# Kernel tuning notes

Measured on AMD Instinct MI355X. Metric: run time of the kernel, lower is better.

Reference implementation:

```python
import jax, jax.numpy as jnp
import numpy as np

V = 32          # num_variables
T = 48          # num_time_bins
D = 512         # d_model
H = 8           # num_heads
HD = D // H     # head_dim = 64
OD = 16         # observation_dim
B = 4


def setup_inputs() -> dict:
    key = jax.random.key(0)
    ks = jax.random.split(key, 20)
    s = 0.02
    inp = {
        'h': jax.random.normal(ks[0], (B, T, V, D), jnp.float32),
        'observation_state': jax.random.normal(ks[1], (B, T, V, 2), jnp.float32),
        'Wq': jax.random.normal(ks[2], (D, D), jnp.float32) * s,
        'bq': jnp.zeros((D,), jnp.float32),
        'Wk': jax.random.normal(ks[3], (D, D), jnp.float32) * s,
        'bk': jnp.zeros((D,), jnp.float32),
        'Wv': jax.random.normal(ks[4], (D, D), jnp.float32) * s,
        'bv': jnp.zeros((D,), jnp.float32),
        'Wo': jax.random.normal(ks[5], (D, D), jnp.float32) * s,
        'bo': jnp.zeros((D,), jnp.float32),
        'Woq': jax.random.normal(ks[6], (2, H * OD), jnp.float32) * 0.5,
        'boq': jnp.zeros((H * OD,), jnp.float32),
        'Wok': jax.random.normal(ks[7], (2, H * OD), jnp.float32) * 0.5,
        'bok': jnp.zeros((H * OD,), jnp.float32),
        'variable_bias': jax.random.normal(ks[8], (H, V, V), jnp.float32) * 0.01,
        'relative_time_bias': jax.random.normal(ks[9], (H, 2 * T - 1), jnp.float32) * 0.01,
    }
    return inp


def reference(h, observation_state, Wq, bq, Wk, bk, Wv, bv, Wo, bo,
              Woq, boq, Wok, bok, variable_bias, relative_time_bias):
    N = T * V
    scale = 1.0 / np.sqrt(HD)
    obs_scale = 1.0 / np.sqrt(OD)

    # static index buffers (constants)
    flat_var_ids = jnp.tile(jnp.arange(V), T)                       # [N]
    flat_time_ids = jnp.repeat(jnp.arange(T), V)                    # [N]
    rel_index = flat_time_ids[:, None] - flat_time_ids[None, :] + (T - 1)  # [N,N]

    fh = h.reshape(B, N, D)
    fo = observation_state.reshape(B, N, 2)

    def heads(x, nh, hd):
        return x.reshape(B, N, nh, hd).transpose(0, 2, 1, 3)  # [B,H,N,hd]

    q = heads(fh @ Wq + bq, H, HD)
    k = heads(fh @ Wk + bk, H, HD)
    v = heads(fh @ Wv + bv, H, HD)
    oq = heads(fo @ Woq + boq, H, OD)
    ok = heads(fo @ Wok + bok, H, OD)

    content = jnp.einsum('bhnd,bhmd->bhnm', q, k) * scale
    obs = jnp.einsum('bhnd,bhmd->bhnm', oq, ok) * obs_scale
    var_scores = variable_bias[:, flat_var_ids[:, None], flat_var_ids[None, :]]  # [H,N,N]
    time_scores = relative_time_bias[:, rel_index]                                # [H,N,N]

    scores = content + obs + var_scores[None] + time_scores[None]
    attn = jax.nn.softmax(scores, axis=-1)  # dropout off (inference)
    out = jnp.einsum('bhnm,bhmd->bhnd', attn, v)
    out = out.transpose(0, 2, 1, 3).reshape(B, N, D)
    out = out @ Wo + bo
    return out.reshape(B, T, V, D)
```

## Files before the change

### kernel.cpp

```cpp
#include <hip/hip_runtime.h>
#include <math.h>

typedef __bf16 bf16x8 __attribute__((ext_vector_type(8)));
typedef float f32x4 __attribute__((ext_vector_type(4)));

#define NB 4
#define NT 48
#define NV 32
#define ND 512
#define NH 8
#define NN 1536
#define NBN 6144
#define L2E 1.44269504f

#define GLOAD_LDS(g, l) \
    __builtin_amdgcn_global_load_lds( \
        (const __attribute__((address_space(1))) void*)(g), \
        (__attribute__((address_space(3))) void*)(l), 16, 0, 0)

__global__ __launch_bounds__(256) void prep(
    const float* __restrict__ h, const float* __restrict__ obs,
    const float* __restrict__ Wq, const float* __restrict__ Wk,
    const float* __restrict__ Wv, const float* __restrict__ Wo,
    const float* __restrict__ bq, const float* __restrict__ bk,
    const float* __restrict__ bv,
    const float* __restrict__ Wok, const float* __restrict__ bok,
    __bf16* __restrict__ h_bf, __bf16* __restrict__ WcatT,
    __bf16* __restrict__ WoT, float* __restrict__ biascat,
    __bf16* __restrict__ kx)
{
    __shared__ float ts[64][68];
    const int tid = threadIdx.x;
    const int bx = blockIdx.x;
    if (bx < 1536) {
        int t = bx * 256 + tid;
        const float4* src = (const float4*)h + (size_t)t * 2;
        float4 a = src[0], b = src[1];
        __bf16 r[8] = {(__bf16)a.x, (__bf16)a.y, (__bf16)a.z, (__bf16)a.w,
                       (__bf16)b.x, (__bf16)b.y, (__bf16)b.z, (__bf16)b.w};
        *(uint4*)(h_bf + (size_t)t * 8) = *(uint4*)r;
    } else if (bx < 1792) {
        int bw = bx - 1536;
        const int p = bw >> 6, tile = bw & 63;
        const int k0 = (tile >> 3) * 64, c0 = (tile & 7) * 64;
        const float* W = (p == 0) ? Wq : (p == 1) ? Wk : (p == 2) ? Wv : Wo;
        const float scale = (p == 0) ? 0.125f * L2E : 1.0f;
        #pragma unroll
        for (int i = 0; i < 4; i++) {
            int r = (tid >> 4) + i * 16;
            float4 v = *(const float4*)(W + (size_t)(k0 + r) * 512 + c0 + (tid & 15) * 4);
            *(float4*)&ts[r][(tid & 15) * 4] = v;
        }
        __syncthreads();
        __bf16 tmp[16];
        #pragma unroll
        for (int j = 0; j < 16; j++)
            tmp[j] = (__bf16)(ts[(tid & 3) * 16 + j][tid >> 2] * scale);
        int crow = c0 + (tid >> 2);
        __bf16* dst = (p < 3)
            ? WcatT + ((size_t)(p * 512 + crow)) * 512 + k0 + (tid & 3) * 16
            : WoT   + ((size_t)crow) * 512 + k0 + (tid & 3) * 16;
        *(uint4*)dst = *(uint4*)tmp;
        *(uint4*)(dst + 8) = *(uint4*)(tmp + 8);
        if (p < 3 && k0 == 0 && tid < 64) {
            const float* bb = (p == 0) ? bq : (p == 1) ? bk : bv;
            biascat[p * 512 + c0 + tid] = bb[c0 + tid] * scale;
        }
    } else {
        int t = (bx - 1792) * 256 + tid;
        int row = t >> 1, half = t & 1;
        __bf16* dst = kx + (size_t)row * 96 + 64 + half * 16;
        if (half == 0) {
            int bh = row / NN, n = row - bh * NN;
            int b = bh >> 3, hh = bh & 7;
            size_t bn = (size_t)b * NN + n;
            float o0 = obs[bn * 2], o1 = obs[bn * 2 + 1];
            int f = hh * 16;
            __bf16 tmp[16];
            #pragma unroll
            for (int j = 0; j < 16; j++)
                tmp[j] = (__bf16)(o0 * Wok[f + j] + o1 * Wok[128 + f + j] + bok[f + j]);
            *(uint4*)dst       = *(uint4*)tmp;
            *(uint4*)(dst + 8) = *(uint4*)(tmp + 8);
        } else {
            uint4 z = {0, 0, 0, 0};
            *(uint4*)dst       = z;
            *(uint4*)(dst + 8) = z;
        }
    }
}

template<int TM, bool BF16OUT>
__global__ __launch_bounds__(256) void gemm_mfma(
    const __bf16* __restrict__ A, const __bf16* __restrict__ Bt,
    const float* __restrict__ bias, float* __restrict__ Cf,
    __bf16* __restrict__ qarr, __bf16* __restrict__ kx,
    __bf16* __restrict__ vt)
{
    constexpr int MT = TM / 32;
    __shared__ __align__(16) char smem[34816];
    __bf16 (*As)[32] = (__bf16(*)[32])smem;
    __bf16 (*Bs)[32] = (__bf16(*)[32])(smem + TM * 64);
    const int tid = threadIdx.x;
    const int w = tid >> 6, lane = tid & 63;
    const int quad = lane >> 4, l16 = lane & 15;
    const int wm = w >> 1, wn = w & 1;
    const int n0 = blockIdx.x * 128, m0 = blockIdx.y * TM;

    const int sm = tid >> 2;
    const int sk = ((tid & 3) ^ ((sm >> 1) & 3)) * 8;
    const __bf16* aptr = A  + (size_t)(m0 + sm) * 512 + sk;
    const __bf16* bptr = Bt + (size_t)(n0 + sm) * 512 + sk;
    __bf16* lA = (__bf16*)As + tid * 8;
    __bf16* lB = (__bf16*)Bs + tid * 8;

    f32x4 zero4 = {0.f, 0.f, 0.f, 0.f};
    f32x4 acc[MT][4];
    #pragma unroll
    for (int i = 0; i < MT; i++)
        #pragma unroll
        for (int j = 0; j < 4; j++) acc[i][j] = zero4;

    for (int kt = 0; kt < 512; kt += 32) {
        __syncthreads();
        GLOAD_LDS(aptr + kt, lA);
        if (TM == 128) GLOAD_LDS(aptr + 64 * 512 + kt, lA + 2048);
        GLOAD_LDS(bptr + kt, lB);
        GLOAD_LDS(bptr + 64 * 512 + kt, lB + 2048);
        __syncthreads();
        bf16x8 af[MT], bfr[4];
        #pragma unroll
        for (int mt = 0; mt < MT; mt++) {
            int rr = wm * (TM / 2) + mt * 16 + l16;
            af[mt] = *(const bf16x8*)&As[rr][(quad ^ ((rr >> 1) & 3)) * 8];
        }
        #pragma unroll
        for (int nt = 0; nt < 4; nt++) {
            int rr = wn * 64 + nt * 16 + l16;
            bfr[nt] = *(const bf16x8*)&Bs[rr][(quad ^ ((rr >> 1) & 3)) * 8];
        }
        #pragma unroll
        for (int mt = 0; mt < MT; mt++)
            #pragma unroll
            for (int nt = 0; nt < 4; nt++)
                acc[mt][nt] = __builtin_amdgcn_mfma_f32_16x16x32_bf16(
                    af[mt], bfr[nt], acc[mt][nt], 0, 0, 0);
    }

    __syncthreads();
    if (BF16OUT) {
        if (n0 >= 1024) {
            __bf16* CsT = (__bf16*)smem;
            #pragma unroll
            for (int nt = 0; nt < 4; nt++) {
                int cl = wn * 64 + nt * 16 + l16;
                float bia = bias[n0 + cl];
                #pragma unroll
                for (int mt = 0; mt < MT; mt++) {
                    int rl0 = wm * (TM / 2) + mt * 16 + quad * 4;
                    __bf16 pk[4];
                    #pragma unroll
                    for (int r = 0; r < 4; r++)
                        pk[r] = (__bf16)(acc[mt][nt][r] + bia);
                    *(uint2*)&CsT[cl * 136 + rl0] = *(uint2*)pk;
                }
            }
            __syncthreads();
            int cl = tid >> 1, half = tid & 1;
            int f0 = (n0 + cl) & 511;
            int hh = f0 >> 6, d = f0 & 63;
            int bidx = m0 / NN, nm = m0 - bidx * NN;
            __bf16* dst = vt + ((size_t)(bidx * 8 + hh) * 64 + d) * 1536
                             + nm + half * 64;
            #pragma unroll
            for (int j = 0; j < 8; j++) {
                uint4 v = *(uint4*)&CsT[cl * 136 + half * 64 + j * 8];
                *(uint4*)(dst + j * 8) = v;
            }
        } else {
            __bf16* Cs = (__bf16*)smem;
            #pragma unroll
            for (int mt = 0; mt < MT; mt++)
                #pragma unroll
                for (int nt = 0; nt < 4; nt++) {
                    int cl = wn * 64 + nt * 16 + l16;
                    float bia = bias[n0 + cl];
                    #pragma unroll
                    for (int r = 0; r < 4; r++) {
                        int rl = wm * (TM / 2) + mt * 16 + quad * 4 + r;
                        Cs[rl * 132 + cl] = (__bf16)(acc[mt][nt][r] + bia);
                    }
                }
            __syncthreads();
            int rl = tid >> 1, hb = tid & 1;
            int grow = m0 + rl;
            int col0 = n0 + hb * 64;
            int p = col0 >> 9, f0 = col0 & 511, hh = f0 >> 6;
            int bidx = grow / NN, n = grow - bidx * NN;
            __bf16* dst = (p == 0) ? qarr + (size_t)grow * 512 + f0
                                   : kx + ((size_t)(bidx * 8 + hh) * NN + n) * 96;
            #pragma unroll
            for (int j = 0; j < 8; j++) {
                uint2 lo = *(uint2*)&Cs[rl * 132 + hb * 64 + j * 8];
                uint2 hi = *(uint2*)&Cs[rl * 132 + hb * 64 + j * 8 + 4];
                uint4 v = {lo.x, lo.y, hi.x, hi.y};
                *(uint4*)(dst + j * 8) = v;
            }
        }
    } else {
        float* Csf = (float*)smem;
        #pragma unroll
        for (int mt = 0; mt < MT; mt++)
            #pragma unroll
            for (int nt = 0; nt < 4; nt++) {
                int cl = wn * 64 + nt * 16 + l16;
                float bia = bias[n0 + cl];
                #pragma unroll
                for (int r = 0; r < 4; r++) {
                    int rl = wm * (TM / 2) + mt * 16 + quad * 4 + r;
                    Csf[rl * 132 + cl] = acc[mt][nt][r] + bia;
                }
            }
        __syncthreads();
        int rl = tid >> 2, q4 = tid & 3;
        float* dst = Cf + (size_t)(m0 + rl) * 512 + n0 + q4 * 32;
        #pragma unroll
        for (int j = 0; j < 8; j++) {
            uint4 v = *(uint4*)&Csf[rl * 132 + q4 * 32 + j * 4];
            *(uint4*)(dst + j * 4) = v;
        }
    }
}

__global__ __launch_bounds__(256) void attn_mfma(
    const __bf16* __restrict__ qarr, const __bf16* __restrict__ kx,
    const __bf16* __restrict__ vt, const float* __restrict__ obs,
    const float* __restrict__ Woq, const float* __restrict__ boq,
    const float* __restrict__ varb, const float* __restrict__ rtb,
    __bf16* __restrict__ aout)
{
    __shared__ __align__(16) __bf16 Ks[64][128];
    __shared__ __align__(16) __bf16 Vs[64][64];
    __shared__ __align__(16) __bf16 Ps[64][64];
    __shared__ float rts[96];

    const int tid = threadIdx.x;
    const int w = tid >> 6, lane = tid & 63;
    const int quad = lane >> 4, l16 = lane & 15;
    const int bh = blockIdx.x, qt = blockIdx.y;
    const int b = bh >> 3, h = bh & 7;
    const int n0 = qt * 64;

    if (tid < 95) rts[tid] = rtb[h * 95 + tid] * L2E;

    const int nl = w * 16 + l16;
    const size_t qrow = (size_t)(b * NN + n0 + nl);
    bf16x8 bq_[3];
    bq_[0] = *(const bf16x8*)(qarr + qrow * 512 + h * 64 + quad * 8);
    bq_[1] = *(const bf16x8*)(qarr + qrow * 512 + h * 64 + 32 + quad * 8);
    {
        uint4 a2u = {0u, 0u, 0u, 0u};
        if (quad < 2) {
            float o0 = obs[qrow * 2], o1 = obs[qrow * 2 + 1];
            int f = h * 16 + quad * 8;
            const float sc = 0.25f * L2E;
            __bf16 tmp[8];
            #pragma unroll
            for (int j = 0; j < 8; j++)
                tmp[j] = (__bf16)(sc * (o0 * Woq[f + j] + o1 * Woq[128 + f + j]
                                        + boq[f + j]));
            a2u = *(uint4*)tmp;
        }
        bq_[2] = *(bf16x8*)&a2u;
    }

    const int rm = (w & 1) * 16 + l16;
    float4 vbA = *(const float4*)(varb + h * 1024 + rm * 32 + quad * 4);
    float4 vbB = *(const float4*)(varb + h * 1024 + rm * 32 + 16 + quad * 4);
    float vA[4] = {vbA.x * L2E, vbA.y * L2E, vbA.z * L2E, vbA.w * L2E};
    float vB[4] = {vbB.x * L2E, vbB.y * L2E, vbB.z * L2E, vbB.w * L2E};
    const int tn = 2 * qt + (w >> 1);

    const int ck = (tid & 15) ^ ((tid >> 4) & 7);
    const __bf16* kbase = kx + (size_t)bh * NN * 96 + ck * 8;
    const int cv = (tid & 7) ^ ((tid >> 3) & 7);
    const __bf16* vbase = vt + (size_t)bh * 64 * 1536 + cv * 8;

    int wo2[4], ro2[2];
    #pragma unroll
    for (int ct = 0; ct < 4; ct++)
        wo2[ct] = (((ct * 2 + (quad >> 1)) ^ (nl & 7)) * 16) + (quad & 1) * 8;
    #pragma unroll
    for (int ks = 0; ks < 2; ks++)
        ro2[ks] = ((ks * 4 + quad) ^ (nl & 7)) * 16;
    char* psrow = (char*)Ps + nl * 128;

    f32x4 zero4 = {0.f, 0.f, 0.f, 0.f};
    f32x4 o[4];
    float lp = 0.f;
    #pragma unroll
    for (int i = 0; i < 4; i++) o[i] = zero4;

    char* ldsK = (char*)Ks;
    char* ldsV = (char*)Vs;

    for (int mt = 0; mt < 24; mt++) {
        const int m0 = mt * 64;
        __syncthreads();
        #pragma unroll
        for (int i = 0; i < 4; i++) {
            int row = i * 16 + (tid >> 4);
            GLOAD_LDS(kbase + (size_t)(m0 + row) * 96, ldsK + i * 4096 + tid * 16);
        }
        #pragma unroll
        for (int i = 0; i < 2; i++) {
            int row = i * 32 + (tid >> 3);
            GLOAD_LDS(vbase + (size_t)row * 1536 + m0, ldsV + i * 4096 + tid * 16);
        }
        __syncthreads();

        f32x4 sc[4];
        #pragma unroll
        for (int ct = 0; ct < 4; ct++) {
            f32x4 d = zero4;
            int row = ct * 16 + l16;
            #pragma unroll
            for (int ks = 0; ks < 3; ks++) {
                bf16x8 kf = *(const bf16x8*)((const char*)Ks + row * 256
                                + (((ks * 4 + quad) ^ (row & 7)) * 16));
                d = __builtin_amdgcn_mfma_f32_16x16x32_bf16(kf, bq_[ks], d, 0, 0, 0);
            }
            sc[ct] = d;
        }
        float tb0 = rts[tn - 2 * mt + 47];
        float tb1 = rts[tn - 2 * mt + 46];
        #pragma unroll
        for (int ct = 0; ct < 4; ct++) {
            float tb = (ct & 2) ? tb1 : tb0;
            const float* vv = (ct & 1) ? vB : vA;
            __bf16 pk[4];
            #pragma unroll
            for (int r = 0; r < 4; r++) {
                float p = exp2f(sc[ct][r] + tb + vv[r]);
                lp += p;
                pk[r] = (__bf16)p;
            }
            *(uint2*)(psrow + wo2[ct]) = *(uint2*)pk;
        }
        #pragma unroll
        for (int ks = 0; ks < 2; ks++) {
            bf16x8 pf = *(const bf16x8*)(psrow + ro2[ks]);
            #pragma unroll
            for (int dt = 0; dt < 4; dt++) {
                int rw = dt * 16 + l16;
                bf16x8 vf = *(const bf16x8*)((const char*)Vs + rw * 128
                                + (((ks * 4 + quad) ^ (rw & 7)) * 16));
                o[dt] = __builtin_amdgcn_mfma_f32_16x16x32_bf16(vf, pf, o[dt], 0, 0, 0);
            }
        }
    }

    lp += __shfl_xor(lp, 16);
    lp += __shfl_xor(lp, 32);
    float inv = 1.0f / lp;
    size_t abase = ((size_t)b * NN + n0 + nl) * 512 + h * 64 + quad * 4;
    #pragma unroll
    for (int dt = 0; dt < 4; dt++) {
        __bf16 ov[4];
        #pragma unroll
        for (int r = 0; r < 4; r++) ov[r] = (__bf16)(o[dt][r] * inv);
        *(uint2*)(aout + abase + dt * 16) = *(uint2*)ov;
    }
}

extern "C" void kernel_launch(void* const* d_in, const int* in_sizes, int n_in,
                              void* d_out, int out_size, void* d_ws, size_t ws_size,
                              hipStream_t stream)
{
    const float* h_   = (const float*)d_in[0];
    const float* obs  = (const float*)d_in[1];
    const float* Wq   = (const float*)d_in[2];
    const float* bq   = (const float*)d_in[3];
    const float* Wk   = (const float*)d_in[4];
    const float* bk   = (const float*)d_in[5];
    const float* Wv   = (const float*)d_in[6];
    const float* bv   = (const float*)d_in[7];
    const float* Wo   = (const float*)d_in[8];
    const float* bo   = (const float*)d_in[9];
    const float* Woq  = (const float*)d_in[10];
    const float* boq  = (const float*)d_in[11];
    const float* Wok  = (const float*)d_in[12];
    const float* bok  = (const float*)d_in[13];
    const float* varb = (const float*)d_in[14];
    const float* rtb  = (const float*)d_in[15];
    float* out = (float*)d_out;

    char* ws = (char*)d_ws;
    __bf16* h_bf    = (__bf16*)ws;                 ws += (size_t)NBN * 512 * 2;
    __bf16* qarr    = (__bf16*)ws;                 ws += (size_t)NBN * 512 * 2;
    __bf16* vt      = (__bf16*)ws;                 ws += (size_t)NBN * 512 * 2;
    __bf16* kx      = (__bf16*)ws;                 ws += ((size_t)32 * NN * 96 + 64) * 2;
    __bf16* attnout = (__bf16*)ws;                 ws += (size_t)NBN * 512 * 2;
    __bf16* WcatT   = (__bf16*)ws;                 ws += (size_t)1536 * 512 * 2;
    __bf16* WoT     = (__bf16*)ws;                 ws += (size_t)512 * 512 * 2;
    float*  biascat = (float*)ws;                  ws += 1536 * 4;

    prep<<<dim3(2176), dim3(256), 0, stream>>>(
        h_, obs, Wq, Wk, Wv, Wo, bq, bk, bv, Wok, bok,
        h_bf, WcatT, WoT, biascat, kx);
    gemm_mfma<128, true><<<dim3(12, 48), dim3(256), 0, stream>>>(
        h_bf, WcatT, biascat, nullptr, qarr, kx, vt);
    attn_mfma<<<dim3(32, 24), dim3(256), 0, stream>>>(qarr, kx, vt, obs, Woq, boq,
                                                      varb, rtb, attnout);
    gemm_mfma<64, false><<<dim3(4, 96), dim3(256), 0, stream>>>(
        attnout, WoT, bo, out, nullptr, nullptr, nullptr);
}
```

Before: 179.7 us.

## Register-prefetch next tiles instead of direct global-to-LDS loads; shrink QKV GEMM tile

Replaces the global_load_lds copies in both the GEMM and attention kernels with loads into registers that fetch the next K-step tile while the current LDS tile is consumed, then store to LDS at the top of the next iteration. The QKV projection GEMM also moves from 128-row to 64-row tiles, doubling the grid to 12x96 blocks, and its epilogue indexing is adjusted to match. The aim is to overlap global memory latency with MFMA work and to improve occupancy and load balance. In exchange it uses more registers, adds LDS store instructions, and loses the per-block reuse that the larger M tile gave.

Result: slower. 263.7 us (+46.7%).

```diff
diff --git a/kernel.cpp b/kernel.cpp
--- a/kernel.cpp
+++ b/kernel.cpp
@@ -12,11 +12,6 @@
 #define NN 1536
 #define NBN 6144
 #define L2E 1.44269504f
-
-#define GLOAD_LDS(g, l) \
-    __builtin_amdgcn_global_load_lds( \
-        (const __attribute__((address_space(1))) void*)(g), \
-        (__attribute__((address_space(3))) void*)(l), 16, 0, 0)
 
 __global__ __launch_bounds__(256) void prep(
     const float* __restrict__ h, const float* __restrict__ obs,
@@ -90,22 +85,21 @@
     }
 }
 
-template<int TM, bool BF16OUT>
+template<bool BF16OUT>
 __global__ __launch_bounds__(256) void gemm_mfma(
     const __bf16* __restrict__ A, const __bf16* __restrict__ Bt,
     const float* __restrict__ bias, float* __restrict__ Cf,
     __bf16* __restrict__ qarr, __bf16* __restrict__ kx,
     __bf16* __restrict__ vt)
 {
-    constexpr int MT = TM / 32;
     __shared__ __align__(16) char smem[34816];
     __bf16 (*As)[32] = (__bf16(*)[32])smem;
-    __bf16 (*Bs)[32] = (__bf16(*)[32])(smem + TM * 64);
+    __bf16 (*Bs)[32] = (__bf16(*)[32])(smem + 4096);
     const int tid = threadIdx.x;
     const int w = tid >> 6, lane = tid & 63;
     const int quad = lane >> 4, l16 = lane & 15;
     const int wm = w >> 1, wn = w & 1;
-    const int n0 = blockIdx.x * 128, m0 = blockIdx.y * TM;
+    const int n0 = blockIdx.x * 128, m0 = blockIdx.y * 64;
 
     const int sm = tid >> 2;
     const int sk = ((tid & 3) ^ ((sm >> 1) & 3)) * 8;
@@ -115,23 +109,31 @@
     __bf16* lB = (__bf16*)Bs + tid * 8;
 
     f32x4 zero4 = {0.f, 0.f, 0.f, 0.f};
-    f32x4 acc[MT][4];
-    #pragma unroll
-    for (int i = 0; i < MT; i++)
+    f32x4 acc[2][4];
+    #pragma unroll
+    for (int i = 0; i < 2; i++)
         #pragma unroll
         for (int j = 0; j < 4; j++) acc[i][j] = zero4;
 
+    uint4 areg = *(const uint4*)aptr;
+    uint4 breg0 = *(const uint4*)bptr;
+    uint4 breg1 = *(const uint4*)(bptr + 64 * 512);
+
     for (int kt = 0; kt < 512; kt += 32) {
         __syncthreads();
-        GLOAD_LDS(aptr + kt, lA);
-        if (TM == 128) GLOAD_LDS(aptr + 64 * 512 + kt, lA + 2048);
-        GLOAD_LDS(bptr + kt, lB);
-        GLOAD_LDS(bptr + 64 * 512 + kt, lB + 2048);
-        __syncthreads();
-        bf16x8 af[MT], bfr[4];
-        #pragma unroll
-        for (int mt = 0; mt < MT; mt++) {
-            int rr = wm * (TM / 2) + mt * 16 + l16;
+        *(uint4*)lA = areg;
+        *(uint4*)lB = breg0;
+        *(uint4*)(lB + 2048) = breg1;
+        __syncthreads();
+        if (kt < 480) {
+            areg  = *(const uint4*)(aptr + kt + 32);
+            breg0 = *(const uint4*)(bptr + kt + 32);
+            breg1 = *(const uint4*)(bptr + 64 * 512 + kt + 32);
+        }
+        bf16x8 af[2], bfr[4];
+        #pragma unroll
+        for (int mt = 0; mt < 2; mt++) {
+            int rr = wm * 32 + mt * 16 + l16;
             af[mt] = *(const bf16x8*)&As[rr][(quad ^ ((rr >> 1) & 3)) * 8];
         }
         #pragma unroll
@@ -140,7 +142,7 @@
             bfr[nt] = *(const bf16x8*)&Bs[rr][(quad ^ ((rr >> 1) & 3)) * 8];
         }
         #pragma unroll
-        for (int mt = 0; mt < MT; mt++)
+        for (int mt = 0; mt < 2; mt++)
             #pragma unroll
             for (int nt = 0; nt < 4; nt++)
                 acc[mt][nt] = __builtin_amdgcn_mfma_f32_16x16x32_bf16(
@@ -156,13 +158,13 @@
                 int cl = wn * 64 + nt * 16 + l16;
                 float bia = bias[n0 + cl];
                 #pragma unroll
-                for (int mt = 0; mt < MT; mt++) {
-                    int rl0 = wm * (TM / 2) + mt * 16 + quad * 4;
+                for (int mt = 0; mt < 2; mt++) {
+                    int rl0 = wm * 32 + mt * 16 + quad * 4;
                     __bf16 pk[4];
                     #pragma unroll
                     for (int r = 0; r < 4; r++)
                         pk[r] = (__bf16)(acc[mt][nt][r] + bia);
-                    *(uint2*)&CsT[cl * 136 + rl0] = *(uint2*)pk;
+                    *(uint2*)&CsT[cl * 72 + rl0] = *(uint2*)pk;
                 }
             }
             __syncthreads();
@@ -171,38 +173,39 @@
             int hh = f0 >> 6, d = f0 & 63;
             int bidx = m0 / NN, nm = m0 - bidx * NN;
             __bf16* dst = vt + ((size_t)(bidx * 8 + hh) * 64 + d) * 1536
-                             + nm + half * 64;
-            #pragma unroll
-            for (int j = 0; j < 8; j++) {
-                uint4 v = *(uint4*)&CsT[cl * 136 + half * 64 + j * 8];
+                             + nm + half * 32;
+            #pragma unroll
+            for (int j = 0; j < 4; j++) {
+                uint4 v = *(uint4*)&CsT[cl * 72 + half * 32 + j * 8];
                 *(uint4*)(dst + j * 8) = v;
             }
         } else {
             __bf16* Cs = (__bf16*)smem;
             #pragma unroll
-            for (int mt = 0; mt < MT; mt++)
+            for (int mt = 0; mt < 2; mt++)
                 #pragma unroll
                 for (int nt = 0; nt < 4; nt++) {
                     int cl = wn * 64 + nt * 16 + l16;
                     float bia = bias[n0 + cl];
                     #pragma unroll
                     for (int r = 0; r < 4; r++) {
-                        int rl = wm * (TM / 2) + mt * 16 + quad * 4 + r;
+                        int rl = wm * 32 + mt * 16 + quad * 4 + r;
                         Cs[rl * 132 + cl] = (__bf16)(acc[mt][nt][r] + bia);
                     }
                 }
             __syncthreads();
-            int rl = tid >> 1, hb = tid & 1;
+            int rl = tid >> 2, hb = tid & 3;
             int grow = m0 + rl;
-            int col0 = n0 + hb * 64;
+            int col0 = n0 + hb * 32;
             int p = col0 >> 9, f0 = col0 & 511, hh = f0 >> 6;
             int bidx = grow / NN, n = grow - bidx * NN;
             __bf16* dst = (p == 0) ? qarr + (size_t)grow * 512 + f0
-                                   : kx + ((size_t)(bidx * 8 + hh) * NN + n) * 96;
-            #pragma unroll
-            for (int j = 0; j < 8; j++) {
-                uint2 lo = *(uint2*)&Cs[rl * 132 + hb * 64 + j * 8];
-                uint2 hi = *(uint2*)&Cs[rl * 132 + hb * 64 + j * 8 + 4];
+                                   : kx + ((size_t)(bidx * 8 + hh) * NN + n) * 96
+                                        + (f0 & 63);
+            #pragma unroll
+            for (int j = 0; j < 4; j++) {
+                uint2 lo = *(uint2*)&Cs[rl * 132 + hb * 32 + j * 8];
+                uint2 hi = *(uint2*)&Cs[rl * 132 + hb * 32 + j * 8 + 4];
                 uint4 v = {lo.x, lo.y, hi.x, hi.y};
                 *(uint4*)(dst + j * 8) = v;
             }
@@ -210,14 +213,14 @@
     } else {
         float* Csf = (float*)smem;
         #pragma unroll
-        for (int mt = 0; mt < MT; mt++)
+        for (int mt = 0; mt < 2; mt++)
             #pragma unroll
             for (int nt = 0; nt < 4; nt++) {
                 int cl = wn * 64 + nt * 16 + l16;
                 float bia = bias[n0 + cl];
                 #pragma unroll
                 for (int r = 0; r < 4; r++) {
-                    int rl = wm * (TM / 2) + mt * 16 + quad * 4 + r;
+                    int rl = wm * 32 + mt * 16 + quad * 4 + r;
                     Csf[rl * 132 + cl] = acc[mt][nt][r] + bia;
                 }
             }
@@ -304,20 +307,40 @@
     char* ldsK = (char*)Ks;
     char* ldsV = (char*)Vs;
 
+    uint4 kreg[4], vreg[2];
+    #pragma unroll
+    for (int i = 0; i < 4; i++) {
+        int row = i * 16 + (tid >> 4);
+        kreg[i] = *(const uint4*)(kbase + (size_t)row * 96);
+    }
+    #pragma unroll
+    for (int i = 0; i < 2; i++) {
+        int row = i * 32 + (tid >> 3);
+        vreg[i] = *(const uint4*)(vbase + (size_t)row * 1536);
+    }
+
     for (int mt = 0; mt < 24; mt++) {
-        const int m0 = mt * 64;
-        __syncthreads();
-        #pragma unroll
-        for (int i = 0; i < 4; i++) {
-            int row = i * 16 + (tid >> 4);
-            GLOAD_LDS(kbase + (size_t)(m0 + row) * 96, ldsK + i * 4096 + tid * 16);
-        }
-        #pragma unroll
-        for (int i = 0; i < 2; i++) {
-            int row = i * 32 + (tid >> 3);
-            GLOAD_LDS(vbase + (size_t)row * 1536 + m0, ldsV + i * 4096 + tid * 16);
-        }
-        __syncthreads();
+        __syncthreads();
+        #pragma unroll
+        for (int i = 0; i < 4; i++)
+            *(uint4*)(ldsK + i * 4096 + tid * 16) = kreg[i];
+        #pragma unroll
+        for (int i = 0; i < 2; i++)
+            *(uint4*)(ldsV + i * 4096 + tid * 16) = vreg[i];
+        __syncthreads();
+        if (mt < 23) {
+            const int m0n = (mt + 1) * 64;
+            #pragma unroll
+            for (int i = 0; i < 4; i++) {
+                int row = m0n + i * 16 + (tid >> 4);
+                kreg[i] = *(const uint4*)(kbase + (size_t)row * 96);
+            }
+            #pragma unroll
+            for (int i = 0; i < 2; i++) {
+                int row = i * 32 + (tid >> 3);
+                vreg[i] = *(const uint4*)(vbase + (size_t)row * 1536 + m0n);
+            }
+        }
 
         f32x4 sc[4];
         #pragma unroll
@@ -408,10 +431,10 @@
     prep<<<dim3(2176), dim3(256), 0, stream>>>(
         h_, obs, Wq, Wk, Wv, Wo, bq, bk, bv, Wok, bok,
         h_bf, WcatT, WoT, biascat, kx);
-    gemm_mfma<128, true><<<dim3(12, 48), dim3(256), 0, stream>>>(
+    gemm_mfma<true><<<dim3(12, 96), dim3(256), 0, stream>>>(
         h_bf, WcatT, biascat, nullptr, qarr, kx, vt);
     attn_mfma<<<dim3(32, 24), dim3(256), 0, stream>>>(qarr, kx, vt, obs, Woq, boq,
                                                       varb, rtb, attnout);
-    gemm_mfma<64, false><<<dim3(4, 96), dim3(256), 0, stream>>>(
+    gemm_mfma<false><<<dim3(4, 96), dim3(256), 0, stream>>>(
         attnout, WoT, bo, out, nullptr, nullptr, nullptr);
 }
```

## Store K and V in MFMA fragment order and load directly from global

Applied to the files above, without the earlier changes.

The projection GEMM and prep kernel now write K (plus observation features) and V in a fragment-major layout matching the MFMA operand register order. The attention kernel drops the per-tile LDS staging of K/V and its barriers, reading each fragment straight from global memory with 16-byte loads. The time bias is also read from global instead of shared memory. This removes LDS traffic and two syncs per tile, but gives up sharing between waves, so each wave refetches K/V through cache and there is no explicit prefetch to hide global latency.

Result: slower. 206.2 us (+14.8%).

```diff
diff --git a/kernel.cpp b/kernel.cpp
--- a/kernel.cpp
+++ b/kernel.cpp
@@ -17,6 +17,7 @@
     __builtin_amdgcn_global_load_lds( \
         (const __attribute__((address_space(1))) void*)(g), \
         (__attribute__((address_space(3))) void*)(l), 16, 0, 0)
+
 
 __global__ __launch_bounds__(256) void prep(
     const float* __restrict__ h, const float* __restrict__ obs,
@@ -27,7 +28,7 @@
     const float* __restrict__ Wok, const float* __restrict__ bok,
     __bf16* __restrict__ h_bf, __bf16* __restrict__ WcatT,
     __bf16* __restrict__ WoT, float* __restrict__ biascat,
-    __bf16* __restrict__ kx)
+    __bf16* __restrict__ kx2)
 {
     __shared__ float ts[64][68];
     const int tid = threadIdx.x;
@@ -68,24 +69,27 @@
         }
     } else {
         int t = (bx - 1792) * 256 + tid;
-        int row = t >> 1, half = t & 1;
-        __bf16* dst = kx + (size_t)row * 96 + 64 + half * 16;
-        if (half == 0) {
-            int bh = row / NN, n = row - bh * NN;
+        int r = t & 15;
+        int c = 8 + ((t >> 4) & 3);
+        int grow = t >> 6;
+        __bf16* dst = kx2 + ((size_t)grow * 12 + c) * 128 + r * 8;
+        if (c < 10) {
+            int bh = grow / 96;
+            int g = grow - bh * 96;
             int b = bh >> 3, hh = bh & 7;
+            int n = g * 16 + r;
             size_t bn = (size_t)b * NN + n;
             float o0 = obs[bn * 2], o1 = obs[bn * 2 + 1];
-            int f = hh * 16;
-            __bf16 tmp[16];
-            #pragma unroll
-            for (int j = 0; j < 16; j++)
-                tmp[j] = (__bf16)(o0 * Wok[f + j] + o1 * Wok[128 + f + j] + bok[f + j]);
-            *(uint4*)dst       = *(uint4*)tmp;
-            *(uint4*)(dst + 8) = *(uint4*)(tmp + 8);
+            int f0 = hh * 16 + (c - 8) * 8;
+            __bf16 tmp[8];
+            #pragma unroll
+            for (int j = 0; j < 8; j++)
+                tmp[j] = (__bf16)(o0 * Wok[f0 + j] + o1 * Wok[128 + f0 + j]
+                                  + bok[f0 + j]);
+            *(uint4*)dst = *(uint4*)tmp;
         } else {
             uint4 z = {0, 0, 0, 0};
-            *(uint4*)dst       = z;
-            *(uint4*)(dst + 8) = z;
+            *(uint4*)dst = z;
         }
     }
 }
@@ -94,8 +98,8 @@
 __global__ __launch_bounds__(256) void gemm_mfma(
     const __bf16* __restrict__ A, const __bf16* __restrict__ Bt,
     const float* __restrict__ bias, float* __restrict__ Cf,
-    __bf16* __restrict__ qarr, __bf16* __restrict__ kx,
-    __bf16* __restrict__ vt)
+    __bf16* __restrict__ qarr, __bf16* __restrict__ kx2,
+    __bf16* __restrict__ vt2)
 {
     constexpr int MT = TM / 32;
     __shared__ __align__(16) char smem[34816];
@@ -170,12 +174,13 @@
             int f0 = (n0 + cl) & 511;
             int hh = f0 >> 6, d = f0 & 63;
             int bidx = m0 / NN, nm = m0 - bidx * NN;
-            __bf16* dst = vt + ((size_t)(bidx * 8 + hh) * 64 + d) * 1536
-                             + nm + half * 64;
+            size_t vg = ((size_t)(bidx * 8 + hh) * 4 + (d >> 4)) * 192
+                      + (nm >> 3) + half * 8;
+            __bf16* dst = vt2 + (vg * 16 + (d & 15)) * 8;
             #pragma unroll
             for (int j = 0; j < 8; j++) {
                 uint4 v = *(uint4*)&CsT[cl * 136 + half * 64 + j * 8];
-                *(uint4*)(dst + j * 8) = v;
+                *(uint4*)(dst + (size_t)j * 128) = v;
             }
         } else {
             __bf16* Cs = (__bf16*)smem;
@@ -197,14 +202,25 @@
             int col0 = n0 + hb * 64;
             int p = col0 >> 9, f0 = col0 & 511, hh = f0 >> 6;
             int bidx = grow / NN, n = grow - bidx * NN;
-            __bf16* dst = (p == 0) ? qarr + (size_t)grow * 512 + f0
-                                   : kx + ((size_t)(bidx * 8 + hh) * NN + n) * 96;
-            #pragma unroll
-            for (int j = 0; j < 8; j++) {
-                uint2 lo = *(uint2*)&Cs[rl * 132 + hb * 64 + j * 8];
-                uint2 hi = *(uint2*)&Cs[rl * 132 + hb * 64 + j * 8 + 4];
-                uint4 v = {lo.x, lo.y, hi.x, hi.y};
-                *(uint4*)(dst + j * 8) = v;
+            if (p == 0) {
+                __bf16* dst = qarr + (size_t)grow * 512 + f0;
+                #pragma unroll
+                for (int j = 0; j < 8; j++) {
+                    uint2 lo = *(uint2*)&Cs[rl * 132 + hb * 64 + j * 8];
+                    uint2 hi = *(uint2*)&Cs[rl * 132 + hb * 64 + j * 8 + 4];
+                    uint4 v = {lo.x, lo.y, hi.x, hi.y};
+                    *(uint4*)(dst + j * 8) = v;
+                }
+            } else {
+                size_t bh96g = (size_t)(bidx * 8 + hh) * 96 + (n >> 4);
+                __bf16* dst = kx2 + bh96g * 1536 + (n & 15) * 8;
+                #pragma unroll
+                for (int j = 0; j < 8; j++) {
+                    uint2 lo = *(uint2*)&Cs[rl * 132 + hb * 64 + j * 8];
+                    uint2 hi = *(uint2*)&Cs[rl * 132 + hb * 64 + j * 8 + 4];
+                    uint4 v = {lo.x, lo.y, hi.x, hi.y};
+                    *(uint4*)(dst + (size_t)j * 128) = v;
+                }
             }
         }
     } else {
@@ -233,16 +249,13 @@
 }
 
 __global__ __launch_bounds__(256) void attn_mfma(
-    const __bf16* __restrict__ qarr, const __bf16* __restrict__ kx,
-    const __bf16* __restrict__ vt, const float* __restrict__ obs,
+    const __bf16* __restrict__ qarr, const __bf16* __restrict__ kx2,
+    const __bf16* __restrict__ vt2, const float* __restrict__ obs,
     const float* __restrict__ Woq, const float* __restrict__ boq,
     const float* __restrict__ varb, const float* __restrict__ rtb,
     __bf16* __restrict__ aout)
 {
-    __shared__ __align__(16) __bf16 Ks[64][128];
-    __shared__ __align__(16) __bf16 Vs[64][64];
     __shared__ __align__(16) __bf16 Ps[64][64];
-    __shared__ float rts[96];
 
     const int tid = threadIdx.x;
     const int w = tid >> 6, lane = tid & 63;
@@ -250,8 +263,6 @@
     const int bh = blockIdx.x, qt = blockIdx.y;
     const int b = bh >> 3, h = bh & 7;
     const int n0 = qt * 64;
-
-    if (tid < 95) rts[tid] = rtb[h * 95 + tid] * L2E;
 
     const int nl = w * 16 + l16;
     const size_t qrow = (size_t)(b * NN + n0 + nl);
@@ -280,11 +291,10 @@
     float vA[4] = {vbA.x * L2E, vbA.y * L2E, vbA.z * L2E, vbA.w * L2E};
     float vB[4] = {vbB.x * L2E, vbB.y * L2E, vbB.z * L2E, vbB.w * L2E};
     const int tn = 2 * qt + (w >> 1);
-
-    const int ck = (tid & 15) ^ ((tid >> 4) & 7);
-    const __bf16* kbase = kx + (size_t)bh * NN * 96 + ck * 8;
-    const int cv = (tid & 7) ^ ((tid >> 3) & 7);
-    const __bf16* vbase = vt + (size_t)bh * 64 * 1536 + cv * 8;
+    const float* rtbh = rtb + h * 95 + tn + 47;
+
+    const __bf16* kfb = kx2 + (size_t)bh * 147456 + quad * 128 + l16 * 8;
+    const __bf16* vfb = vt2 + (size_t)bh * 98304  + quad * 128 + l16 * 8;
 
     int wo2[4], ro2[2];
     #pragma unroll
@@ -301,47 +311,24 @@
     #pragma unroll
     for (int i = 0; i < 4; i++) o[i] = zero4;
 
-    char* ldsK = (char*)Ks;
-    char* ldsV = (char*)Vs;
-
     for (int mt = 0; mt < 24; mt++) {
-        const int m0 = mt * 64;
-        __syncthreads();
-        #pragma unroll
-        for (int i = 0; i < 4; i++) {
-            int row = i * 16 + (tid >> 4);
-            GLOAD_LDS(kbase + (size_t)(m0 + row) * 96, ldsK + i * 4096 + tid * 16);
-        }
-        #pragma unroll
-        for (int i = 0; i < 2; i++) {
-            int row = i * 32 + (tid >> 3);
-            GLOAD_LDS(vbase + (size_t)row * 1536 + m0, ldsV + i * 4096 + tid * 16);
-        }
-        __syncthreads();
-
-        f32x4 sc[4];
+        float tb0 = rtbh[-2 * mt] * L2E;
+        float tb1 = rtbh[-2 * mt - 1] * L2E;
         #pragma unroll
         for (int ct = 0; ct < 4; ct++) {
             f32x4 d = zero4;
-            int row = ct * 16 + l16;
             #pragma unroll
             for (int ks = 0; ks < 3; ks++) {
-                bf16x8 kf = *(const bf16x8*)((const char*)Ks + row * 256
-                                + (((ks * 4 + quad) ^ (row & 7)) * 16));
+                bf16x8 kf = *(const bf16x8*)(kfb
+                    + (((size_t)(mt * 4 + ct) * 12 + ks * 4) << 7));
                 d = __builtin_amdgcn_mfma_f32_16x16x32_bf16(kf, bq_[ks], d, 0, 0, 0);
             }
-            sc[ct] = d;
-        }
-        float tb0 = rts[tn - 2 * mt + 47];
-        float tb1 = rts[tn - 2 * mt + 46];
-        #pragma unroll
-        for (int ct = 0; ct < 4; ct++) {
             float tb = (ct & 2) ? tb1 : tb0;
             const float* vv = (ct & 1) ? vB : vA;
             __bf16 pk[4];
             #pragma unroll
             for (int r = 0; r < 4; r++) {
-                float p = exp2f(sc[ct][r] + tb + vv[r]);
+                float p = exp2f(d[r] + tb + vv[r]);
                 lp += p;
                 pk[r] = (__bf16)p;
             }
@@ -352,9 +339,8 @@
             bf16x8 pf = *(const bf16x8*)(psrow + ro2[ks]);
             #pragma unroll
             for (int dt = 0; dt < 4; dt++) {
-                int rw = dt * 16 + l16;
-                bf16x8 vf = *(const bf16x8*)((const char*)Vs + rw * 128
-                                + (((ks * 4 + quad) ^ (rw & 7)) * 16));
+                bf16x8 vf = *(const bf16x8*)(vfb
+                    + (((size_t)dt * 192 + mt * 8 + ks * 4) << 7));
                 o[dt] = __builtin_amdgcn_mfma_f32_16x16x32_bf16(vf, pf, o[dt], 0, 0, 0);
             }
         }
@@ -398,19 +384,19 @@
     char* ws = (char*)d_ws;
     __bf16* h_bf    = (__bf16*)ws;                 ws += (size_t)NBN * 512 * 2;
     __bf16* qarr    = (__bf16*)ws;                 ws += (size_t)NBN * 512 * 2;
-    __bf16* vt      = (__bf16*)ws;                 ws += (size_t)NBN * 512 * 2;
-    __bf16* kx      = (__bf16*)ws;                 ws += ((size_t)32 * NN * 96 + 64) * 2;
+    __bf16* vt2     = (__bf16*)ws;                 ws += (size_t)NBN * 512 * 2;
+    __bf16* kx2     = (__bf16*)ws;                 ws += (size_t)32 * 96 * 12 * 128 * 2;
     __bf16* attnout = (__bf16*)ws;                 ws += (size_t)NBN * 512 * 2;
     __bf16* WcatT   = (__bf16*)ws;                 ws += (size_t)1536 * 512 * 2;
     __bf16* WoT     = (__bf16*)ws;                 ws += (size_t)512 * 512 * 2;
     float*  biascat = (float*)ws;                  ws += 1536 * 4;
 
-    prep<<<dim3(2176), dim3(256), 0, stream>>>(
+    prep<<<dim3(2560), dim3(256), 0, stream>>>(
         h_, obs, Wq, Wk, Wv, Wo, bq, bk, bv, Wok, bok,
-        h_bf, WcatT, WoT, biascat, kx);
+        h_bf, WcatT, WoT, biascat, kx2);
     gemm_mfma<128, true><<<dim3(12, 48), dim3(256), 0, stream>>>(
-        h_bf, WcatT, biascat, nullptr, qarr, kx, vt);
-    attn_mfma<<<dim3(32, 24), dim3(256), 0, stream>>>(qarr, kx, vt, obs, Woq, boq,
+        h_bf, WcatT, biascat, nullptr, qarr, kx2, vt2);
+    attn_mfma<<<dim3(32, 24), dim3(256), 0, stream>>>(qarr, kx2, vt2, obs, Woq, boq,
                                                       varb, rtb, attnout);
     gemm_mfma<64, false><<<dim3(4, 96), dim3(256), 0, stream>>>(
         attnout, WoT, bo, out, nullptr, nullptr, nullptr);
```
